# Kernel optimization log

Measured on AMD Instinct MI355X. Metric: run time of the kernel, lower is better.

Reference implementation:

```python
import jax, jax.numpy as jnp
from jax import lax
import numpy as np

B, E, D, V, NB, R = 512, 128, 8, 50000, 4, 3  # batch, embed/hidden/classes, capsule_length, num_items, num_beh, routing iters
TP, TC, TF, TK = 50, 50, 50, 200  # purchase/cart/fav/click lengths


def setup_inputs() -> dict:
    key = jax.random.key(0)
    k = jax.random.split(key, 12)
    item_emb = jax.random.normal(k[4], (V + 1, E), jnp.float32)
    item_emb = item_emb.at[0].set(0.0)  # padding_idx=0
    return {
        "purchase_seq": jax.random.randint(k[0], (B, TP), 0, V + 1),
        "cart_seq": jax.random.randint(k[1], (B, TC), 0, V + 1),
        "fav_seq": jax.random.randint(k[2], (B, TF), 0, V + 1),
        "click_seq": jax.random.randint(k[3], (B, TK), 0, V + 1),
        "item_emb": item_emb,
        "gru_Wih": 0.1 * jax.random.normal(k[5], (NB, 3 * E, E), jnp.float32),
        "gru_Whh": 0.1 * jax.random.normal(k[6], (NB, 3 * E, E), jnp.float32),
        "gru_bih": jnp.zeros((NB, 3 * E), jnp.float32),
        "gru_bhh": jnp.zeros((NB, 3 * E), jnp.float32),
        "W": 0.01 * jax.random.uniform(k[7], (E, NB, E, D), dtype=jnp.float32),
        "w_scale": jnp.ones((E,), jnp.float32),
        "bias_vec": jnp.zeros((E,), jnp.float32),
        "alpha": jnp.full((1,), float(E), jnp.float32),
        "W_coef": 0.1 * jax.random.normal(k[8], (E, E + D, D), jnp.float32),
    }


def _gru_last(x, Wih, Whh, bih, bhh):
    """Standard GRU over x: (B, T, E); returns final hidden state (B, H)."""
    H = Whh.shape[1]

    def step(h, xt):
        gi = xt @ Wih.T + bih
        gh = h @ Whh.T + bhh
        ir, iz, inn = jnp.split(gi, 3, axis=-1)
        hr, hz, hn = jnp.split(gh, 3, axis=-1)
        r = jax.nn.sigmoid(ir + hr)
        z = jax.nn.sigmoid(iz + hz)
        n = jnp.tanh(inn + r * hn)
        return (1.0 - z) * n + z * h, None

    h0 = jnp.zeros((x.shape[0], H), x.dtype)
    h, _ = lax.scan(step, h0, jnp.swapaxes(x, 0, 1))
    return h


def _forward(seqs, item_emb, gru_Wih, gru_Whh, gru_bih, gru_bhh, W, w_scale, bias_vec, alpha, W_coef):
    hs = []
    for i, s in enumerate(seqs):  # fixed small loop over num_beh=4 structurally distinct GRUs
        emb = item_emb[s] * (s != 0)[..., None].astype(item_emb.dtype)
        hs.append(_gru_last(emb, gru_Wih[i], gru_Whh[i], gru_bih[i], gru_bhh[i]))
    e = jnp.stack(hs, axis=-1)  # (B, H, NB)  == stack(dim=1).permute(0,2,1)
    u = jnp.einsum('bht,htcd->bhcd', e, W)  # (B, H, C, D)
    b = jnp.zeros(u.shape[:3] + (1,), u.dtype)
    u_det = lax.stop_gradient(u)
    E_det = lax.stop_gradient(item_emb)
    for _ in range(R - 1):  # detached routing-by-agreement iterations
        c = jax.nn.softmax(b, axis=2)
        v = lax.stop_gradient(alpha) * jnp.sum(c * u_det, axis=1)  # (B, C, D)
        v_ = jnp.linalg.norm(v, axis=-1) * lax.stop_gradient(w_scale) + lax.stop_gradient(bias_vec)  # (B, C)
        p = jax.nn.softmax(v_ @ E_det.T, axis=-1) @ E_det  # (B, E) soft vocab lookup
        p = jnp.broadcast_to(p[:, None, :], (p.shape[0], u.shape[2], p.shape[-1]))  # (B, C, E)
        coef = jnp.einsum('bcd,cdD->bcD', jnp.concatenate([p, v], axis=-1), W_coef)  # (B, C, D)
        b = b + jnp.sum(u_det * coef[:, None], axis=-1, keepdims=True)
    c = jax.nn.softmax(b, axis=2)
    v = alpha * jnp.sum(c * u, axis=1)
    v_ = jnp.linalg.norm(v, axis=-1) * w_scale + bias_vec
    return v_ @ item_emb.T  # (B, V+1)


def reference(purchase_seq, cart_seq, fav_seq, click_seq, item_emb, gru_Wih, gru_Whh, gru_bih, gru_bhh, W, w_scale, bias_vec, alpha, W_coef):
    return _forward((purchase_seq, cart_seq, fav_seq, click_seq), item_emb, gru_Wih, gru_Whh,
                    gru_bih, gru_bhh, W, w_scale, bias_vec, alpha, W_coef)
```

## Files before the change

kernel.cpp:

```cpp
#include <hip/hip_runtime.h>
#include <math.h>

typedef __attribute__((ext_vector_type(8))) short bf16x8;
typedef __attribute__((ext_vector_type(4))) float f32x4;
typedef __attribute__((ext_vector_type(2))) float f32x2;
typedef __attribute__((ext_vector_type(4))) unsigned short u16x4;
typedef __attribute__((ext_vector_type(4))) _Float16 f16x4;
typedef __attribute__((ext_vector_type(8))) _Float16 f16x8;

static __device__ __forceinline__ short f2bf(float f) {
  unsigned u = __builtin_bit_cast(unsigned, f);
  u += 0x7fffu + ((u >> 16) & 1u);
  return (short)(u >> 16);
}
static __device__ __forceinline__ float bf2f(unsigned short s) {
  unsigned u = ((unsigned)s) << 16;
  return __builtin_bit_cast(float, u);
}
static __device__ __forceinline__ f32x4 mfma16(bf16x8 a, bf16x8 b, f32x4 c) {
  return __builtin_amdgcn_mfma_f32_16x16x32_bf16(a, b, c, 0, 0, 0);
}
static __device__ __forceinline__ bf16x8 pack8v(f32x4 a, f32x4 b) {
  bf16x8 r;
  r[0]=f2bf(a[0]); r[1]=f2bf(a[1]); r[2]=f2bf(a[2]); r[3]=f2bf(a[3]);
  r[4]=f2bf(b[0]); r[5]=f2bf(b[1]); r[6]=f2bf(b[2]); r[7]=f2bf(b[3]);
  return r;
}
static __device__ __forceinline__ float fastrcp(float x) {
  float r;
  asm("v_rcp_f32_e32 %0, %1" : "=v"(r) : "v"(x));
  return r;
}
static __device__ __forceinline__ float dot4(f32x4 a, f32x4 b) {
  return a[0]*b[0] + a[1]*b[1] + a[2]*b[2] + a[3]*b[3];
}

#define LGKM_BARRIER() do {                                   \
    asm volatile("s_waitcnt lgkmcnt(0)" ::: "memory");        \
    __builtin_amdgcn_s_barrier();                             \
    __builtin_amdgcn_sched_barrier(0);                        \
  } while (0)

__global__ __launch_bounds__(512) void gi_gemm_kernel(
    const int* __restrict__ seq0, const int* __restrict__ seq1,
    const int* __restrict__ seq2, const int* __restrict__ seq3,
    const float* __restrict__ item_emb, const float* __restrict__ Wih,
    unsigned short* __restrict__ gi_t50, unsigned short* __restrict__ gi_click)
{
  const int b = blockIdx.x;
  int beh, tile0;
  if (b < 100)      { beh = 0; tile0 = b * 16; }
  else if (b < 200) { beh = 1; tile0 = (b - 100) * 16; }
  else if (b < 300) { beh = 2; tile0 = (b - 200) * 16; }
  else              { beh = 3; tile0 = (b - 300) * 16; }
  const int T = (beh == 3) ? 200 : 50;
  const int* seq = (beh == 0) ? seq0 : (beh == 1) ? seq1 : (beh == 2) ? seq2 : seq3;
  unsigned short* gibase = (beh == 3) ? gi_click : (gi_t50 + (size_t)beh * 9830400);

  const int tid = threadIdx.x;
  const int wave = tid >> 6, lane = tid & 63, lrow = lane & 15, lk8 = lane >> 4;
  const int bcol = wave * 16 + lrow;

  bf16x8 wif[3][4];
  const float* WihB = Wih + (size_t)beh * 384 * 128;
#pragma unroll
  for (int g = 0; g < 3; ++g) {
    const int wr = g * 128 + bcol;
#pragma unroll
    for (int kt = 0; kt < 4; ++kt) {
      const int k0 = kt * 32 + lk8 * 8;
      f32x4 a0 = *(const f32x4*)(WihB + (size_t)wr * 128 + k0);
      f32x4 a1 = *(const f32x4*)(WihB + (size_t)wr * 128 + k0 + 4);
      wif[g][kt] = pack8v(a0, a1);
    }
  }

  __shared__ short xt[16][132];
  const int gj = tid >> 5;
  const int gc = (tid & 31) * 4;

  for (int ti = 0; ti < 16; ++ti) {
    const int tile = tile0 + ti;
    const int r0blk = tile / T;
    const int t = tile - r0blk * T;
    {
      const int sidx = seq[(size_t)(r0blk * 16 + gj) * T + t];
      const f32x4 xv = *(const f32x4*)(item_emb + (size_t)sidx * 128 + gc);
      xt[gj][gc]     = f2bf(xv[0]);
      xt[gj][gc + 1] = f2bf(xv[1]);
      xt[gj][gc + 2] = f2bf(xv[2]);
      xt[gj][gc + 3] = f2bf(xv[3]);
    }
    __syncthreads();
    bf16x8 ax[4];
#pragma unroll
    for (int kt = 0; kt < 4; ++kt)
      ax[kt] = *(const bf16x8*)&xt[lrow][kt * 32 + lk8 * 8];
    f32x4 acc[3] = {{0,0,0,0},{0,0,0,0},{0,0,0,0}};
#pragma unroll
    for (int kt = 0; kt < 4; ++kt) {
      acc[0] = mfma16(ax[kt], wif[0][kt], acc[0]);
      acc[1] = mfma16(ax[kt], wif[1][kt], acc[1]);
      acc[2] = mfma16(ax[kt], wif[2][kt], acc[2]);
    }
    unsigned short* base = gibase + ((size_t)(r0blk * 4 + lk8) * T + t) * 1536;
    unsigned short* dst = base + bcol * 4;
#pragma unroll
    for (int g = 0; g < 3; ++g) {
      u16x4 o;
      o[0] = (unsigned short)f2bf(acc[g][0]);
      o[1] = (unsigned short)f2bf(acc[g][1]);
      o[2] = (unsigned short)f2bf(acc[g][2]);
      o[3] = (unsigned short)f2bf(acc[g][3]);
      *(u16x4*)(dst + g * 512) = o;
    }
    __syncthreads();
  }
}

__global__ __launch_bounds__(256, 2) void gru_rec5w_kernel(
    const float* __restrict__ Whh, const float* __restrict__ bih,
    const float* __restrict__ bhh,
    const unsigned short* __restrict__ gi_t50,
    const unsigned short* __restrict__ gi_click,
    const float* __restrict__ item_emb, short* __restrict__ Et,
    float* __restrict__ e_out)
{
  __shared__ short h0[16][140];
  __shared__ short h1[16][140];
  __shared__ float ttile[64][36];
  const int tid = threadIdx.x;

  if (blockIdx.x >= 512) {
    const int wb = blockIdx.x - 512;
    for (int unit = wb; unit < 3128; unit += 128) {
      const int vt = unit >> 2, kp = unit & 3;
      const int v0 = vt * 64, ks = kp * 32;
      const int r = tid >> 2, cc = (tid & 3) * 8;
      f32x4 x0 = {0,0,0,0}, x1 = {0,0,0,0};
      if (v0 + r < 50001) {
        x0 = *(const f32x4*)(item_emb + (size_t)(v0 + r) * 128 + ks + cc);
        x1 = *(const f32x4*)(item_emb + (size_t)(v0 + r) * 128 + ks + cc + 4);
      }
      *(f32x4*)&ttile[r][cc] = x0;
      *(f32x4*)&ttile[r][cc + 4] = x1;
      __syncthreads();
      const int k = tid >> 3, vs = (tid & 7) * 8;
#pragma unroll
      for (int j = 0; j < 8; j += 4) {
        u16x4 o;
        o[0] = (unsigned short)f2bf(ttile[vs + j][k]);
        o[1] = (unsigned short)f2bf(ttile[vs + j + 1][k]);
        o[2] = (unsigned short)f2bf(ttile[vs + j + 2][k]);
        o[3] = (unsigned short)f2bf(ttile[vs + j + 3][k]);
        *(u16x4*)((unsigned short*)Et + (size_t)(ks + k) * 50048 + v0 + vs + j) = o;
      }
      __syncthreads();
    }
    return;
  }

  const int beh = blockIdx.x >> 7;
  const int qt = blockIdx.x & 127;
  const int T = (beh == 3) ? 200 : 50;
  const unsigned short* gib =
      ((beh == 3) ? gi_click : (gi_t50 + (size_t)beh * 9830400)) + (size_t)qt * T * 1536;

  const int w = tid >> 6;
  const int lane = tid & 63;
  const int lrow = lane & 15;
  const int lk8 = lane >> 4;
  const int col0 = w * 32 + lrow;
  const int col1 = col0 + 16;

  bf16x8 whf[3][2][4];
  const float* WhhB = Whh + (size_t)beh * 384 * 128;
#pragma unroll
  for (int g = 0; g < 3; ++g) {
#pragma unroll
    for (int ct = 0; ct < 2; ++ct) {
      const int wr = g * 128 + (ct ? col1 : col0);
#pragma unroll
      for (int kt = 0; kt < 4; ++kt) {
        const int k0 = kt * 32 + lk8 * 8;
        f32x4 b0 = *(const f32x4*)(WhhB + (size_t)wr * 128 + k0);
        f32x4 b1 = *(const f32x4*)(WhhB + (size_t)wr * 128 + k0 + 4);
        whf[g][ct][kt] = pack8v(b0, b1);
      }
    }
  }
  float bR[2], bZ[2], bN[2], bHN[2];
#pragma unroll
  for (int ct = 0; ct < 2; ++ct) {
    const int c = ct ? col1 : col0;
    bR[ct]  = bih[beh * 384 + c] + bhh[beh * 384 + c];
    bZ[ct]  = bih[beh * 384 + 128 + c] + bhh[beh * 384 + 128 + c];
    bN[ct]  = bih[beh * 384 + 256 + c];
    bHN[ct] = bhh[beh * 384 + 256 + c];
  }

  for (int i = tid; i < 16 * 140; i += 256) { ((short*)h0)[i] = 0; ((short*)h1)[i] = 0; }
  float hreg[2] = {0.f, 0.f};
  __syncthreads();

  const unsigned short* gp0 = gib + col0 * 4 + lk8;
  const unsigned short* gp1 = gib + col1 * 4 + lk8;

  unsigned short ga[30], gb[30];

#define LOAD_CHUNK(BUF, C0) do {                                              \
    _Pragma("unroll")                                                         \
    for (int _s = 0; _s < 5; ++_s) {                                          \
      const size_t _o = (size_t)((C0) + _s) * 1536;                           \
      _Pragma("unroll")                                                       \
      for (int _g = 0; _g < 3; ++_g) {                                        \
        BUF[_s * 6 + 0 * 3 + _g] = gp0[_o + _g * 512];                        \
        BUF[_s * 6 + 1 * 3 + _g] = gp1[_o + _g * 512];                        \
      }                                                                       \
    }                                                                         \
  } while (0)

  short (*hin)[140] = h0;
  short (*hout)[140] = h1;

#define STEP(BUF, S) do {                                                     \
    bf16x8 ah[4];                                                             \
    _Pragma("unroll")                                                         \
    for (int kt = 0; kt < 4; ++kt)                                            \
      ah[kt] = *(const bf16x8*)&hin[lrow][kt * 32 + lk8 * 8];                 \
    f32x4 hr_[2], hz_[2], hn_[2];                                             \
    _Pragma("unroll")                                                         \
    for (int ct = 0; ct < 2; ++ct) {                                          \
      hr_[ct] = (f32x4){0,0,0,0}; hz_[ct] = (f32x4){0,0,0,0}; hn_[ct] = (f32x4){0,0,0,0}; \
      _Pragma("unroll")                                                       \
      for (int kt = 0; kt < 4; ++kt) {                                        \
        hr_[ct] = mfma16(ah[kt], whf[0][ct][kt], hr_[ct]);                    \
        hz_[ct] = mfma16(ah[kt], whf[1][ct][kt], hz_[ct]);                    \
        hn_[ct] = mfma16(ah[kt], whf[2][ct][kt], hn_[ct]);                    \
      }                                                                       \
    }                                                                         \
    _Pragma("unroll")                                                         \
    for (int ct = 0; ct < 2; ++ct) {                                          \
      const float xr = bf2f(BUF[(S)*6 + ct*3 + 0]) + bR[ct] + hr_[ct][0];     \
      const float xz = bf2f(BUF[(S)*6 + ct*3 + 1]) + bZ[ct] + hz_[ct][0];     \
      const float ea = __expf(-xr);                                           \
      const float eb = __expf(-xz);                                           \
      const float pa = 1.f + ea, pb = 1.f + eb;                               \
      const float rd = fastrcp(pa * pb);                                      \
      const float rr = pb * rd;                                               \
      const float zz = pa * rd;                                               \
      const float tn = bf2f(BUF[(S)*6 + ct*3 + 2]) + bN[ct] + rr * (hn_[ct][0] + bHN[ct]); \
      const float tt = __expf(-2.f * tn);                                     \
      const float nn = (1.f - tt) * fastrcp(1.f + tt);                        \
      hreg[ct] = nn + zz * (hreg[ct] - nn);                                   \
      hout[lk8 * 4][ct ? col1 : col0] = f2bf(hreg[ct]);                       \
    }                                                                         \
    LGKM_BARRIER();                                                           \
    short (*_tmp)[140] = hin; hin = hout; hout = _tmp;                        \
  } while (0)

  LOAD_CHUNK(ga, 0);
  for (int c = 0; c < T; c += 10) {
    if (c + 5 < T) LOAD_CHUNK(gb, c + 5);
    STEP(ga, 0); STEP(ga, 1); STEP(ga, 2); STEP(ga, 3); STEP(ga, 4);
    if (c + 10 < T) LOAD_CHUNK(ga, c + 10);
    STEP(gb, 0); STEP(gb, 1); STEP(gb, 2); STEP(gb, 3); STEP(gb, 4);
  }
#undef STEP
#undef LOAD_CHUNK

#pragma unroll
  for (int ct = 0; ct < 2; ++ct)
    e_out[(size_t)(qt * 4 + lk8) * 512 + (ct ? col1 : col0) * 4 + beh] = hreg[ct];
}

template<int MODE>
__global__ __launch_bounds__(256, 1) void route_kernel(
    const float* __restrict__ b_old, float* __restrict__ b_new,
    const float* __restrict__ e_buf, const float* __restrict__ W,
    const float* __restrict__ coef_buf,
    const float* __restrict__ w_scale, const float* __restrict__ bias_vec,
    const float* __restrict__ alpha,
    float* __restrict__ v_buf, float* __restrict__ vn_buf)
{
  __shared__ float e_lds[4][128][4];
  __shared__ float vacc[4][4][128][8];
  const int g0 = blockIdx.x * 4;
  const int tid = threadIdx.x;
  const int wv = tid >> 6, ln = tid & 63;
  const int c0 = ln * 2;
  for (int i = tid; i < 2048; i += 256) ((float*)e_lds)[i] = e_buf[(size_t)g0 * 512 + i];

  f32x4 cf[4][2][2];
  if (MODE != 0) {
#pragma unroll
    for (int g = 0; g < 4; ++g)
#pragma unroll
      for (int cc = 0; cc < 2; ++cc) {
        cf[g][cc][0] = *(const f32x4*)(coef_buf + (size_t)(g0 + g) * 1024 + (c0 + cc) * 8);
        cf[g][cc][1] = *(const f32x4*)(coef_buf + (size_t)(g0 + g) * 1024 + (c0 + cc) * 8 + 4);
      }
  }
  __syncthreads();

  f32x4 av[4][2][2];
#pragma unroll
  for (int g = 0; g < 4; ++g)
#pragma unroll
    for (int cc = 0; cc < 2; ++cc) { av[g][cc][0] = (f32x4){0,0,0,0}; av[g][cc][1] = (f32x4){0,0,0,0}; }

  const int hbeg = wv * 32;
  for (int h = hbeg; h < hbeg + 32; ++h) {
    f32x4 wr[4][2][2];
#pragma unroll
    for (int t = 0; t < 4; ++t) {
      const float* wp = W + ((size_t)(h * 4 + t) * 128 + c0) * 8;
      wr[t][0][0] = *(const f32x4*)(wp);
      wr[t][0][1] = *(const f32x4*)(wp + 4);
      wr[t][1][0] = *(const f32x4*)(wp + 8);
      wr[t][1][1] = *(const f32x4*)(wp + 12);
    }
    f32x2 bo[4];
    if (MODE == 2) {
#pragma unroll
      for (int g = 0; g < 4; ++g)
        bo[g] = *(const f32x2*)(b_old + (size_t)(g0 + g) * 16384 + h * 128 + c0);
    }
#pragma unroll
    for (int g = 0; g < 4; ++g) {
      const f32x4 ev = *(const f32x4*)&e_lds[g][h][0];
      f32x4 u[2][2];
#pragma unroll
      for (int cc = 0; cc < 2; ++cc)
#pragma unroll
        for (int dd = 0; dd < 2; ++dd)
          u[cc][dd] = ev[0]*wr[0][cc][dd] + ev[1]*wr[1][cc][dd]
                    + ev[2]*wr[2][cc][dd] + ev[3]*wr[3][cc][dd];
      float cv0, cv1;
      if (MODE == 0) {
        cv0 = 0.0078125f; cv1 = 0.0078125f;
      } else {
        float b0 = dot4(u[0][0], cf[g][0][0]) + dot4(u[0][1], cf[g][0][1]);
        float b1 = dot4(u[1][0], cf[g][1][0]) + dot4(u[1][1], cf[g][1][1]);
        if (MODE == 2) { b0 += bo[g][0]; b1 += bo[g][1]; }
        if (MODE == 1)
          *(f32x2*)(b_new + (size_t)(g0 + g) * 16384 + h * 128 + c0) = (f32x2){b0, b1};
        float m = fmaxf(b0, b1);
#pragma unroll
        for (int off = 32; off > 0; off >>= 1) m = fmaxf(m, __shfl_xor(m, off));
        const float e0 = __expf(b0 - m), e1 = __expf(b1 - m);
        float s = e0 + e1;
#pragma unroll
        for (int off = 32; off > 0; off >>= 1) s += __shfl_xor(s, off);
        const float inv = 1.f / s;
        cv0 = e0 * inv; cv1 = e1 * inv;
      }
      av[g][0][0] += cv0 * u[0][0]; av[g][0][1] += cv0 * u[0][1];
      av[g][1][0] += cv1 * u[1][0]; av[g][1][1] += cv1 * u[1][1];
    }
  }
#pragma unroll
  for (int g = 0; g < 4; ++g)
#pragma unroll
    for (int cc = 0; cc < 2; ++cc) {
      *(f32x4*)&vacc[wv][g][c0 + cc][0] = av[g][cc][0];
      *(f32x4*)&vacc[wv][g][c0 + cc][4] = av[g][cc][1];
    }
  __syncthreads();

  const float al = alpha[0];
  const int rg = tid >> 6;
  const int rc = (tid & 63) * 2;
#pragma unroll
  for (int cc = 0; cc < 2; ++cc) {
    const int c = rc + cc;
    f32x4 s0 = *(const f32x4*)&vacc[0][rg][c][0];
    f32x4 s1 = *(const f32x4*)&vacc[0][rg][c][4];
#pragma unroll
    for (int wq = 1; wq < 4; ++wq) {
      s0 += *(const f32x4*)&vacc[wq][rg][c][0];
      s1 += *(const f32x4*)&vacc[wq][rg][c][4];
    }
    s0 *= al; s1 *= al;
    *(f32x4*)(v_buf + (size_t)(g0 + rg) * 1024 + c * 8) = s0;
    *(f32x4*)(v_buf + (size_t)(g0 + rg) * 1024 + c * 8 + 4) = s1;
    const float ss = dot4(s0, s0) + dot4(s1, s1);
    vn_buf[(g0 + rg) * 128 + c] = sqrtf(ss) * w_scale[c] + bias_vec[c];
  }
}

__global__ __launch_bounds__(512) void logits16s_kernel(
    const float* __restrict__ vn, const float* __restrict__ E,
    _Float16* __restrict__ out16, float* __restrict__ pm, float* __restrict__ ps)
{
  __shared__ short et[64][136];
  const int n0 = blockIdx.x * 64;
  const int tid = threadIdx.x;
  const int wave = tid >> 6, lane = tid & 63, lrow = lane & 15, lk8 = lane >> 4;
  {
    const int r = tid >> 3, ks = (tid & 7) * 16;
    const int v = n0 + r;
    f32x4 a = {0,0,0,0}, b = {0,0,0,0}, c = {0,0,0,0}, d = {0,0,0,0};
    if (v < 50001) {
      const float* p = E + (size_t)v * 128 + ks;
      a = *(const f32x4*)p; b = *(const f32x4*)(p + 4);
      c = *(const f32x4*)(p + 8); d = *(const f32x4*)(p + 12);
    }
    *(bf16x8*)&et[r][ks] = pack8v(a, b);
    *(bf16x8*)&et[r][ks + 8] = pack8v(c, d);
  }
  __syncthreads();
  for (int mb = 0; mb < 4; ++mb) {
    const int m0 = mb * 128;
    const int arow = m0 + wave * 16 + lrow;
    bf16x8 afr[4];
#pragma unroll
    for (int kt = 0; kt < 4; ++kt) {
      const float* p = vn + (size_t)arow * 128 + kt * 32 + lk8 * 8;
      afr[kt] = pack8v(*(const f32x4*)p, *(const f32x4*)(p + 4));
    }
    f32x4 acc[4] = {{0,0,0,0},{0,0,0,0},{0,0,0,0},{0,0,0,0}};
#pragma unroll
    for (int kt = 0; kt < 4; ++kt) {
#pragma unroll
      for (int nt = 0; nt < 4; ++nt) {
        const bf16x8 bfr = *(const bf16x8*)&et[nt * 16 + lrow][kt * 32 + lk8 * 8];
        acc[nt] = mfma16(afr[kt], bfr, acc[nt]);
      }
    }
    float xv[4][4];
#pragma unroll
    for (int nt = 0; nt < 4; ++nt) {
      const int col = n0 + nt * 16 + lrow;
      const int row = m0 + wave * 16 + lk8 * 4;
#pragma unroll
      for (int e2 = 0; e2 < 4; ++e2) {
        const float v = (col < 50001) ? acc[nt][e2] : -60000.f;
        const _Float16 h16 = (_Float16)v;
        out16[(size_t)(row + e2) * 50048 + col] = h16;
        xv[e2][nt] = (float)h16;
      }
    }
#pragma unroll
    for (int e2 = 0; e2 < 4; ++e2) {
      float lm = fmaxf(fmaxf(xv[e2][0], xv[e2][1]), fmaxf(xv[e2][2], xv[e2][3]));
#pragma unroll
      for (int off = 8; off > 0; off >>= 1) lm = fmaxf(lm, __shfl_xor(lm, off));
      float s = __expf(xv[e2][0] - lm) + __expf(xv[e2][1] - lm)
              + __expf(xv[e2][2] - lm) + __expf(xv[e2][3] - lm);
#pragma unroll
      for (int off = 8; off > 0; off >>= 1) s += __shfl_xor(s, off);
      if (lrow == 0) {
        const int row = m0 + wave * 16 + lk8 * 4 + e2;
        pm[(size_t)row * 784 + blockIdx.x] = lm;
        ps[(size_t)row * 784 + blockIdx.x] = s;
      }
    }
  }
}

__global__ __launch_bounds__(256) void rowstats_p_kernel(
    const float* __restrict__ pm, const float* __restrict__ ps,
    float* __restrict__ row_m, float* __restrict__ row_inv)
{
  const int b = blockIdx.x;
  const int tid = threadIdx.x;
  const float* pmr = pm + (size_t)b * 784;
  const float* psr = ps + (size_t)b * 784;
  __shared__ float sm[4], ssum[4];
  const int wv = tid >> 6, ln = tid & 63;
  float m = -1e30f;
  for (int i = tid; i < 782; i += 256) m = fmaxf(m, pmr[i]);
#pragma unroll
  for (int off = 32; off > 0; off >>= 1) m = fmaxf(m, __shfl_xor(m, off));
  if (ln == 0) sm[wv] = m;
  __syncthreads();
  const float M = fmaxf(fmaxf(sm[0], sm[1]), fmaxf(sm[2], sm[3]));
  float s = 0.f;
  for (int i = tid; i < 782; i += 256) s += psr[i] * __expf(pmr[i] - M);
#pragma unroll
  for (int off = 32; off > 0; off >>= 1) s += __shfl_xor(s, off);
  if (ln == 0) ssum[wv] = s;
  __syncthreads();
  if (tid == 0) {
    row_m[b] = M;
    row_inv[b] = 1.f / (ssum[0] + ssum[1] + ssum[2] + ssum[3]);
  }
}

__global__ __launch_bounds__(256) void pgemm16_kernel(
    const _Float16* __restrict__ lg, const short* __restrict__ Et,
    const float* __restrict__ row_m, const float* __restrict__ row_inv,
    float* __restrict__ p_buf)
{
  const int tid = threadIdx.x;
  const int wave = tid >> 6, lane = tid & 63, lrow = lane & 15, lk8 = lane >> 4;
  const int m0 = blockIdx.y * 64;
  const int row = m0 + wave * 16 + lrow;
  const float rm = row_m[row], ri = row_inv[row];
  const _Float16* lp = lg + (size_t)row * 50048;
  const int kbeg = blockIdx.x * 1024;
  const int kend = (kbeg + 1024 <= 50048) ? kbeg + 1024 : 50048;
  f32x4 acc[8] = {{0,0,0,0},{0,0,0,0},{0,0,0,0},{0,0,0,0},
                  {0,0,0,0},{0,0,0,0},{0,0,0,0},{0,0,0,0}};
  for (int v0 = kbeg; v0 < kend; v0 += 32) {
    const int kb = v0 + lk8 * 8;
    const f16x8 v8 = *(const f16x8*)(lp + kb);
    bf16x8 afr;
#pragma unroll
    for (int j = 0; j < 8; ++j) afr[j] = f2bf(__expf((float)v8[j] - rm) * ri);
#pragma unroll
    for (int nt = 0; nt < 8; ++nt) {
      const bf16x8 bfr = *(const bf16x8*)(Et + (size_t)(nt * 16 + lrow) * 50048 + kb);
      acc[nt] = mfma16(afr, bfr, acc[nt]);
    }
  }
#pragma unroll
  for (int nt = 0; nt < 8; ++nt)
#pragma unroll
    for (int e2 = 0; e2 < 4; ++e2)
      atomicAdd(&p_buf[(size_t)(m0 + wave * 16 + lk8 * 4 + e2) * 128 + nt * 16 + lrow], acc[nt][e2]);
}

__global__ __launch_bounds__(256) void coef_kernel(
    const float* __restrict__ p_buf, const float* __restrict__ v_buf,
    const float* __restrict__ W_coef, float* __restrict__ coef_buf)
{
  __shared__ float p_lds[4][128];
  const int g0 = blockIdx.x * 4;
  const int tid = threadIdx.x;
  for (int i = tid; i < 512; i += 256) ((float*)p_lds)[i] = p_buf[(size_t)g0 * 128 + i];
  __syncthreads();
  const int c = tid >> 1, dh = (tid & 1) * 4;
  float vg[4][8];
#pragma unroll
  for (int g = 0; g < 4; ++g) {
    const f32x4 va = *(const f32x4*)(v_buf + (size_t)(g0 + g) * 1024 + c * 8);
    const f32x4 vb = *(const f32x4*)(v_buf + (size_t)(g0 + g) * 1024 + c * 8 + 4);
    vg[g][0]=va[0]; vg[g][1]=va[1]; vg[g][2]=va[2]; vg[g][3]=va[3];
    vg[g][4]=vb[0]; vg[g][5]=vb[1]; vg[g][6]=vb[2]; vg[g][7]=vb[3];
  }
  const float* wc = W_coef + (size_t)c * 1088 + dh;
  f32x4 acc[4] = {{0,0,0,0},{0,0,0,0},{0,0,0,0},{0,0,0,0}};
  for (int dp = 0; dp < 128; ++dp) {
    const f32x4 w4 = *(const f32x4*)(wc + (size_t)dp * 8);
#pragma unroll
    for (int g = 0; g < 4; ++g) acc[g] += p_lds[g][dp] * w4;
  }
#pragma unroll
  for (int q = 0; q < 8; ++q) {
    const f32x4 w4 = *(const f32x4*)(wc + (size_t)(128 + q) * 8);
#pragma unroll
    for (int g = 0; g < 4; ++g) acc[g] += vg[g][q] * w4;
  }
#pragma unroll
  for (int g = 0; g < 4; ++g)
    *(f32x4*)(coef_buf + (size_t)(g0 + g) * 1024 + c * 8 + dh) = acc[g];
}

__global__ __launch_bounds__(512) void logits32_kernel(
    const float* __restrict__ vn, const float* __restrict__ E,
    float* __restrict__ out)
{
  __shared__ short et[64][136];
  const int n0 = blockIdx.x * 64;
  const int tid = threadIdx.x;
  const int wave = tid >> 6, lane = tid & 63, lrow = lane & 15, lk8 = lane >> 4;
  {
    const int r = tid >> 3, ks = (tid & 7) * 16;
    const int v = n0 + r;
    f32x4 a = {0,0,0,0}, b = {0,0,0,0}, c = {0,0,0,0}, d = {0,0,0,0};
    if (v < 50001) {
      const float* p = E + (size_t)v * 128 + ks;
      a = *(const f32x4*)p; b = *(const f32x4*)(p + 4);
      c = *(const f32x4*)(p + 8); d = *(const f32x4*)(p + 12);
    }
    *(bf16x8*)&et[r][ks] = pack8v(a, b);
    *(bf16x8*)&et[r][ks + 8] = pack8v(c, d);
  }
  __syncthreads();
  for (int mb = 0; mb < 4; ++mb) {
    const int m0 = mb * 128;
    const int arow = m0 + wave * 16 + lrow;
    bf16x8 afr[4];
#pragma unroll
    for (int kt = 0; kt < 4; ++kt) {
      const float* p = vn + (size_t)arow * 128 + kt * 32 + lk8 * 8;
      afr[kt] = pack8v(*(const f32x4*)p, *(const f32x4*)(p + 4));
    }
    f32x4 acc[4] = {{0,0,0,0},{0,0,0,0},{0,0,0,0},{0,0,0,0}};
#pragma unroll
    for (int kt = 0; kt < 4; ++kt) {
#pragma unroll
      for (int nt = 0; nt < 4; ++nt) {
        const bf16x8 bfr = *(const bf16x8*)&et[nt * 16 + lrow][kt * 32 + lk8 * 8];
        acc[nt] = mfma16(afr[kt], bfr, acc[nt]);
      }
    }
#pragma unroll
    for (int nt = 0; nt < 4; ++nt) {
      const int col = n0 + nt * 16 + lrow;
      if (col < 50001) {
        const int row = m0 + wave * 16 + lk8 * 4;
#pragma unroll
        for (int e2 = 0; e2 < 4; ++e2)
          out[(size_t)(row + e2) * 50001 + col] = acc[nt][e2];
      }
    }
  }
}

extern "C" void kernel_launch(void* const* d_in, const int* in_sizes, int n_in,
                              void* d_out, int out_size, void* d_ws, size_t ws_size,
                              hipStream_t stream) {
  const int* seq0 = (const int*)d_in[0];
  const int* seq1 = (const int*)d_in[1];
  const int* seq2 = (const int*)d_in[2];
  const int* seq3 = (const int*)d_in[3];
  const float* item_emb = (const float*)d_in[4];
  const float* Wih = (const float*)d_in[5];
  const float* Whh = (const float*)d_in[6];
  const float* bih = (const float*)d_in[7];
  const float* bhh = (const float*)d_in[8];
  const float* W = (const float*)d_in[9];
  const float* w_scale = (const float*)d_in[10];
  const float* bias_vec = (const float*)d_in[11];
  const float* alpha = (const float*)d_in[12];
  const float* W_coef = (const float*)d_in[13];
  float* out = (float*)d_out;
  _Float16* lg16 = (_Float16*)d_out;

  char* ws = (char*)d_ws;
  float* e_buf    = (float*)(ws);
  float* b_state  = (float*)(ws + 1048576);
  float* v_buf    = (float*)(ws + 34603008);
  float* vn_buf   = (float*)(ws + 36700160);
  float* p_buf    = (float*)(ws + 36962304);
  float* coef_buf = (float*)(ws + 37224448);
  float* row_m    = (float*)(ws + 39321600);
  float* row_inv  = (float*)(ws + 39323648);
  float* pstat_m  = (float*)(ws + 39325696);
  float* pstat_s  = (float*)(ws + 40931328);

  unsigned short* gi_t50   = (unsigned short*)(ws + 1048576);
  unsigned short* gi_click = (unsigned short*)d_out;
  short* Et = (short*)((char*)d_out + 78643200);

  gi_gemm_kernel<<<dim3(700), 512, 0, stream>>>(seq0, seq1, seq2, seq3, item_emb, Wih,
                                                gi_t50, gi_click);
  gru_rec5w_kernel<<<dim3(640), 256, 0, stream>>>(Whh, bih, bhh, gi_t50, gi_click,
                                                  item_emb, Et, e_buf);
  route_kernel<0><<<dim3(128), 256, 0, stream>>>(nullptr, nullptr, e_buf, W, nullptr,
                                                 w_scale, bias_vec, alpha, v_buf, vn_buf);
  logits16s_kernel<<<dim3(782), 512, 0, stream>>>(vn_buf, item_emb, lg16, pstat_m, pstat_s);
  rowstats_p_kernel<<<dim3(512), 256, 0, stream>>>(pstat_m, pstat_s, row_m, row_inv);
  hipMemsetAsync(p_buf, 0, 262144, stream);
  pgemm16_kernel<<<dim3(49, 8), 256, 0, stream>>>(lg16, Et, row_m, row_inv, p_buf);
  coef_kernel<<<dim3(128), 256, 0, stream>>>(p_buf, v_buf, W_coef, coef_buf);
  route_kernel<1><<<dim3(128), 256, 0, stream>>>(nullptr, b_state, e_buf, W, coef_buf,
                                                 w_scale, bias_vec, alpha, v_buf, vn_buf);
  logits16s_kernel<<<dim3(782), 512, 0, stream>>>(vn_buf, item_emb, lg16, pstat_m, pstat_s);
  rowstats_p_kernel<<<dim3(512), 256, 0, stream>>>(pstat_m, pstat_s, row_m, row_inv);
  hipMemsetAsync(p_buf, 0, 262144, stream);
  pgemm16_kernel<<<dim3(49, 8), 256, 0, stream>>>(lg16, Et, row_m, row_inv, p_buf);
  coef_kernel<<<dim3(128), 256, 0, stream>>>(p_buf, v_buf, W_coef, coef_buf);
  route_kernel<2><<<dim3(128), 256, 0, stream>>>(b_state, nullptr, e_buf, W, coef_buf,
                                                 w_scale, bias_vec, alpha, v_buf, vn_buf);
  logits32_kernel<<<dim3(782), 512, 0, stream>>>(vn_buf, item_emb, out);
}
```

Before: 789.4 us.

## Stage fp16 logits through LDS, store routing logits in fp16, retile GEMM grids

Several independent changes. The fp16 logits kernel now stages its tile in shared memory and writes it back as coalesced 16-element row segments instead of scattered 2-byte stores. The routing state b is kept in fp16, halving its write and read traffic. The p_buf memset is folded into rowstats_p, and pgemm16 uses 512-thread blocks covering 128 rows. gi_gemm also launches twice as many blocks with half the tiles each. The fp16 routing state costs some precision, and the extra LDS and barriers add overhead in the logits kernel.

```diff
diff --git a/kernel.cpp b/kernel.cpp
--- a/kernel.cpp
+++ b/kernel.cpp
@@ -5,6 +5,7 @@
 typedef __attribute__((ext_vector_type(4))) float f32x4;
 typedef __attribute__((ext_vector_type(2))) float f32x2;
 typedef __attribute__((ext_vector_type(4))) unsigned short u16x4;
+typedef __attribute__((ext_vector_type(2))) _Float16 f16x2;
 typedef __attribute__((ext_vector_type(4))) _Float16 f16x4;
 typedef __attribute__((ext_vector_type(8))) _Float16 f16x8;
 
@@ -49,10 +50,10 @@
 {
   const int b = blockIdx.x;
   int beh, tile0;
-  if (b < 100)      { beh = 0; tile0 = b * 16; }
-  else if (b < 200) { beh = 1; tile0 = (b - 100) * 16; }
-  else if (b < 300) { beh = 2; tile0 = (b - 200) * 16; }
-  else              { beh = 3; tile0 = (b - 300) * 16; }
+  if (b < 200)      { beh = 0; tile0 = b * 8; }
+  else if (b < 400) { beh = 1; tile0 = (b - 200) * 8; }
+  else if (b < 600) { beh = 2; tile0 = (b - 400) * 8; }
+  else              { beh = 3; tile0 = (b - 600) * 8; }
   const int T = (beh == 3) ? 200 : 50;
   const int* seq = (beh == 0) ? seq0 : (beh == 1) ? seq1 : (beh == 2) ? seq2 : seq3;
   unsigned short* gibase = (beh == 3) ? gi_click : (gi_t50 + (size_t)beh * 9830400);
@@ -79,7 +80,7 @@
   const int gj = tid >> 5;
   const int gc = (tid & 31) * 4;
 
-  for (int ti = 0; ti < 16; ++ti) {
+  for (int ti = 0; ti < 8; ++ti) {
     const int tile = tile0 + ti;
     const int r0blk = tile / T;
     const int t = tile - r0blk * T;
@@ -276,7 +277,7 @@
 
 template<int MODE>
 __global__ __launch_bounds__(256, 1) void route_kernel(
-    const float* __restrict__ b_old, float* __restrict__ b_new,
+    const _Float16* __restrict__ b_old, _Float16* __restrict__ b_new,
     const float* __restrict__ e_buf, const float* __restrict__ W,
     const float* __restrict__ coef_buf,
     const float* __restrict__ w_scale, const float* __restrict__ bias_vec,
@@ -320,11 +321,11 @@
       wr[t][1][0] = *(const f32x4*)(wp + 8);
       wr[t][1][1] = *(const f32x4*)(wp + 12);
     }
-    f32x2 bo[4];
+    f16x2 bo[4];
     if (MODE == 2) {
 #pragma unroll
       for (int g = 0; g < 4; ++g)
-        bo[g] = *(const f32x2*)(b_old + (size_t)(g0 + g) * 16384 + h * 128 + c0);
+        bo[g] = *(const f16x2*)(b_old + (size_t)(g0 + g) * 16384 + h * 128 + c0);
     }
 #pragma unroll
     for (int g = 0; g < 4; ++g) {
@@ -342,9 +343,11 @@
       } else {
         float b0 = dot4(u[0][0], cf[g][0][0]) + dot4(u[0][1], cf[g][0][1]);
         float b1 = dot4(u[1][0], cf[g][1][0]) + dot4(u[1][1], cf[g][1][1]);
-        if (MODE == 2) { b0 += bo[g][0]; b1 += bo[g][1]; }
-        if (MODE == 1)
-          *(f32x2*)(b_new + (size_t)(g0 + g) * 16384 + h * 128 + c0) = (f32x2){b0, b1};
+        if (MODE == 2) { b0 += (float)bo[g][0]; b1 += (float)bo[g][1]; }
+        if (MODE == 1) {
+          f16x2 bw; bw[0] = (_Float16)b0; bw[1] = (_Float16)b1;
+          *(f16x2*)(b_new + (size_t)(g0 + g) * 16384 + h * 128 + c0) = bw;
+        }
         float m = fmaxf(b0, b1);
 #pragma unroll
         for (int off = 32; off > 0; off >>= 1) m = fmaxf(m, __shfl_xor(m, off));
@@ -394,6 +397,7 @@
     _Float16* __restrict__ out16, float* __restrict__ pm, float* __restrict__ ps)
 {
   __shared__ short et[64][136];
+  __shared__ _Float16 st[128][72];
   const int n0 = blockIdx.x * 64;
   const int tid = threadIdx.x;
   const int wave = tid >> 6, lane = tid & 63, lrow = lane & 15, lk8 = lane >> 4;
@@ -432,12 +436,11 @@
 #pragma unroll
     for (int nt = 0; nt < 4; ++nt) {
       const int col = n0 + nt * 16 + lrow;
-      const int row = m0 + wave * 16 + lk8 * 4;
 #pragma unroll
       for (int e2 = 0; e2 < 4; ++e2) {
         const float v = (col < 50001) ? acc[nt][e2] : -60000.f;
         const _Float16 h16 = (_Float16)v;
-        out16[(size_t)(row + e2) * 50048 + col] = h16;
+        st[wave * 16 + lk8 * 4 + e2][nt * 16 + lrow] = h16;
         xv[e2][nt] = (float)h16;
       }
     }
@@ -456,15 +459,26 @@
         ps[(size_t)row * 784 + blockIdx.x] = s;
       }
     }
+    __syncthreads();
+    {
+      const int row = tid >> 2, cseg = (tid & 3) * 16;
+      const f16x8 a = *(const f16x8*)&st[row][cseg];
+      const f16x8 b = *(const f16x8*)&st[row][cseg + 8];
+      _Float16* op = out16 + (size_t)(m0 + row) * 50048 + n0 + cseg;
+      *(f16x8*)op = a;
+      *(f16x8*)(op + 8) = b;
+    }
+    __syncthreads();
   }
 }
 
 __global__ __launch_bounds__(256) void rowstats_p_kernel(
     const float* __restrict__ pm, const float* __restrict__ ps,
-    float* __restrict__ row_m, float* __restrict__ row_inv)
+    float* __restrict__ row_m, float* __restrict__ row_inv, float* __restrict__ p_buf)
 {
   const int b = blockIdx.x;
   const int tid = threadIdx.x;
+  if (tid < 128) p_buf[b * 128 + tid] = 0.f;
   const float* pmr = pm + (size_t)b * 784;
   const float* psr = ps + (size_t)b * 784;
   __shared__ float sm[4], ssum[4];
@@ -488,14 +502,14 @@
   }
 }
 
-__global__ __launch_bounds__(256) void pgemm16_kernel(
+__global__ __launch_bounds__(512) void pgemm16_kernel(
     const _Float16* __restrict__ lg, const short* __restrict__ Et,
     const float* __restrict__ row_m, const float* __restrict__ row_inv,
     float* __restrict__ p_buf)
 {
   const int tid = threadIdx.x;
   const int wave = tid >> 6, lane = tid & 63, lrow = lane & 15, lk8 = lane >> 4;
-  const int m0 = blockIdx.y * 64;
+  const int m0 = blockIdx.y * 128;
   const int row = m0 + wave * 16 + lrow;
   const float rm = row_m[row], ri = row_inv[row];
   const _Float16* lp = lg + (size_t)row * 50048;
@@ -631,8 +645,8 @@
   _Float16* lg16 = (_Float16*)d_out;
 
   char* ws = (char*)d_ws;
-  float* e_buf    = (float*)(ws);
-  float* b_state  = (float*)(ws + 1048576);
+  float* e_buf       = (float*)(ws);
+  _Float16* b_state  = (_Float16*)(ws + 1048576);
   float* v_buf    = (float*)(ws + 34603008);
   float* vn_buf   = (float*)(ws + 36700160);
   float* p_buf    = (float*)(ws + 36962304);
@@ -646,23 +660,21 @@
   unsigned short* gi_click = (unsigned short*)d_out;
   short* Et = (short*)((char*)d_out + 78643200);
 
-  gi_gemm_kernel<<<dim3(700), 512, 0, stream>>>(seq0, seq1, seq2, seq3, item_emb, Wih,
-                                                gi_t50, gi_click);
+  gi_gemm_kernel<<<dim3(1400), 512, 0, stream>>>(seq0, seq1, seq2, seq3, item_emb, Wih,
+                                                 gi_t50, gi_click);
   gru_rec5w_kernel<<<dim3(640), 256, 0, stream>>>(Whh, bih, bhh, gi_t50, gi_click,
                                                   item_emb, Et, e_buf);
   route_kernel<0><<<dim3(128), 256, 0, stream>>>(nullptr, nullptr, e_buf, W, nullptr,
                                                  w_scale, bias_vec, alpha, v_buf, vn_buf);
   logits16s_kernel<<<dim3(782), 512, 0, stream>>>(vn_buf, item_emb, lg16, pstat_m, pstat_s);
-  rowstats_p_kernel<<<dim3(512), 256, 0, stream>>>(pstat_m, pstat_s, row_m, row_inv);
-  hipMemsetAsync(p_buf, 0, 262144, stream);
-  pgemm16_kernel<<<dim3(49, 8), 256, 0, stream>>>(lg16, Et, row_m, row_inv, p_buf);
+  rowstats_p_kernel<<<dim3(512), 256, 0, stream>>>(pstat_m, pstat_s, row_m, row_inv, p_buf);
+  pgemm16_kernel<<<dim3(49, 4), 512, 0, stream>>>(lg16, Et, row_m, row_inv, p_buf);
   coef_kernel<<<dim3(128), 256, 0, stream>>>(p_buf, v_buf, W_coef, coef_buf);
   route_kernel<1><<<dim3(128), 256, 0, stream>>>(nullptr, b_state, e_buf, W, coef_buf,
                                                  w_scale, bias_vec, alpha, v_buf, vn_buf);
   logits16s_kernel<<<dim3(782), 512, 0, stream>>>(vn_buf, item_emb, lg16, pstat_m, pstat_s);
-  rowstats_p_kernel<<<dim3(512), 256, 0, stream>>>(pstat_m, pstat_s, row_m, row_inv);
-  hipMemsetAsync(p_buf, 0, 262144, stream);
-  pgemm16_kernel<<<dim3(49, 8), 256, 0, stream>>>(lg16, Et, row_m, row_inv, p_buf);
+  rowstats_p_kernel<<<dim3(512), 256, 0, stream>>>(pstat_m, pstat_s, row_m, row_inv, p_buf);
+  pgemm16_kernel<<<dim3(49, 4), 512, 0, stream>>>(lg16, Et, row_m, row_inv, p_buf);
   coef_kernel<<<dim3(128), 256, 0, stream>>>(p_buf, v_buf, W_coef, coef_buf);
   route_kernel<2><<<dim3(128), 256, 0, stream>>>(b_state, nullptr, e_buf, W, coef_buf,
                                                  w_scale, bias_vec, alpha, v_buf, vn_buf);
```

Result: slower. 834.8 us (+5.8%).
